# Performance work log

Hardware: AMD Instinct MI355X
Metric: run time of the kernel (lower is better)

The kernel has to match this reference:

```python
import jax, jax.numpy as jnp
import numpy as np

# LIFParameters(thr=0.4, tau=20.0, tau_o=20.0, damp=0.3, n_ref=5)
THR = 0.4
DECAY = float(np.exp(-1.0 / 20.0))   # membrane decay
KAPPA = float(np.exp(-1.0 / 20.0))   # output filter decay
N_REF = 5.0
DAMP = 0.3
SCALE = 1.0                           # scaling_factor

B, NIN, H, NOUT = 1024, 2048, 2048, 512


def setup_inputs() -> dict:
    key = jax.random.key(0)
    ks = jax.random.split(key, 10)
    inputs = (jax.random.uniform(ks[0], (B, NIN)) < 0.1).astype(jnp.float32)   # input spikes
    v = jax.random.uniform(ks[1], (B, H)) * THR                                # membrane potentials
    z = (jax.random.uniform(ks[2], (B, H)) < 0.2).astype(jnp.float32)          # previous spikes
    r = jax.random.randint(ks[3], (B, H), 0, 6).astype(jnp.float32)            # refractory counters
    out = jax.random.normal(ks[4], (B, NOUT)) * 0.1                            # filtered output
    trace_in = jax.random.uniform(ks[5], (B, NIN))
    trace_rec = jax.random.uniform(ks[6], (B, H))
    w_in = jax.random.normal(ks[7], (NIN, H)) / np.sqrt(NIN)
    w_rec = jax.random.normal(ks[8], (H, H)) / np.sqrt(H)
    w_out = jax.random.normal(ks[9], (H, NOUT)) / np.sqrt(H)
    return dict(inputs=inputs, v=v, z=z, r=r, out=out, trace_in=trace_in,
                trace_rec=trace_rec, w_in=w_in, w_rec=w_rec, w_out=w_out)


@jax.custom_vjp
def spike(v_scaled):
    return (v_scaled > 0.0).astype(v_scaled.dtype)

def _spike_fwd(v_scaled):
    return spike(v_scaled), v_scaled

def _spike_bwd(v_scaled, g):
    # surrogate gradient: damp * max(0, 1 - |v_scaled|)
    return (g * DAMP * jnp.maximum(1.0 - jnp.abs(v_scaled), 0.0),)

spike.defvjp(_spike_fwd, _spike_bwd)


def reference(inputs, v, z, r, out, trace_in, trace_rec, w_in, w_rec, w_out):
    # --- lif_step ---
    i_t = inputs @ w_in + z @ w_rec                      # [B,H] synaptic current
    new_v = DECAY * v + i_t - z * THR                    # leaky integration + reset
    v_scaled = (new_v - THR) / THR
    new_z = spike(v_scaled)
    new_z = jnp.where(r > 0.1, 0.0, new_z)               # refractory masking (old r)
    new_r = jnp.clip(r + N_REF * new_z - 1.0, 0.0, N_REF)
    new_out = KAPPA * out + new_z @ (w_out * SCALE)      # [B,NOUT]
    # --- e-prop extras (call_eprop) ---
    dz_dh = jnp.maximum(DAMP * (1.0 - jnp.abs(v_scaled)), 0.0) / THR
    dz_dh = jnp.where(r > 0.1, 0.0, dz_dh)               # zero in refractory period
    new_trace_in = trace_in * DECAY + inputs
    new_trace_rec = trace_rec * DECAY + z
    return (new_out, new_z, new_v, new_r, new_trace_in, new_trace_rec, dz_dh)
```

## Files before the change

### kernel.cpp

```cpp
#include <hip/hip_runtime.h>

#define Bq 1024
#define Hq 2048
#define NOUTq 512

#define DECAYF 0.95122942450071400910f
#define THRF 0.4f
#define SINVF 5931641.0f

#define OFF_OUT  0
#define OFF_Z    524288
#define OFF_V    2621440
#define OFF_R    4718592
#define OFF_TIN  6815744
#define OFF_TREC 8912896
#define OFF_DZ   11010048

#define WS_A     0ul
#define WS_Q0    4194304ul
#define WS_Q1    12582912ul
#define WS_Q2    20971520ul
#define WS_WOUTT 29360128ul
#define WS_P     31457280ul
#define WS_Z2    65011712ul
#define WS_NEED  69206016ul

typedef __attribute__((ext_vector_type(8))) short  bf16x8;
typedef __attribute__((ext_vector_type(4))) short  s16x4;
typedef __attribute__((ext_vector_type(4))) float  f32x4;
typedef __attribute__((ext_vector_type(4))) int    i32x4;
typedef __attribute__((ext_vector_type(4))) char   c8x4;

__device__ __forceinline__ unsigned short cvt_bf16(float f) {
  unsigned u = __float_as_uint(f);
  return (unsigned short)((u + 0x7FFFu + ((u >> 16) & 1u)) >> 16);
}

__device__ __forceinline__ void gl_lds16(const void* g, void* l) {
  __builtin_amdgcn_global_load_lds((const __attribute__((address_space(1))) unsigned int*)g,
                                   (__attribute__((address_space(3))) unsigned int*)l, 16, 0, 0);
}


__global__ __launch_bounds__(256)
void prep(const float* __restrict__ w_in, const float* __restrict__ w_rec,
          const float* __restrict__ w_out, signed char* __restrict__ Q0,
          signed char* __restrict__ Q1, signed char* __restrict__ Q2,
          short* __restrict__ WoutT,
          const f32x4* __restrict__ ins, const f32x4* __restrict__ zin,
          signed char* __restrict__ Acomb)
{
  __shared__ float tile[64][65];
  const int bx = blockIdx.x, tid = threadIdx.x;
  if (bx >= 2304) {
    const int i = (bx - 2304) * 256 + tid;
    const f32x4 b = ins[i];
    const f32x4 d = zin[i];
    const int e = i * 4, m = e >> 11, k = e & 2047;
    c8x4 ab, zb;
#pragma unroll
    for (int j = 0; j < 4; ++j) { ab[j] = (char)(b[j] != 0.0f); zb[j] = (char)(d[j] != 0.0f); }
    *(c8x4*)&Acomb[m * 4096 + k] = ab;
    *(c8x4*)&Acomb[m * 4096 + 2048 + k] = zb;
    return;
  }
  const int rr = tid >> 4, c4 = (tid & 15) * 4;
  if (bx < 2048) {
    const int k0 = (bx >> 5) * 64, n0 = (bx & 31) * 64;
#pragma unroll
    for (int p = 0; p < 4; ++p) {
      const int kk = p * 16 + rr, kg = k0 + kk;
      const float* src = (kg < 2048) ? &w_in[kg * 2048 + n0 + c4]
                                     : &w_rec[(kg - 2048) * 2048 + n0 + c4];
      const f32x4 v = *(const f32x4*)src;
#pragma unroll
      for (int j = 0; j < 4; ++j) tile[kk][c4 + j] = v[j];
    }
    __syncthreads();
#pragma unroll
    for (int p = 0; p < 4; ++p) {
      const int nn = p * 16 + rr;
      c8x4 b0, b1, b2;
#pragma unroll
      for (int j = 0; j < 4; ++j) {
        int q = __float2int_rn(tile[c4 + j][nn] * SINVF);
        const int d2 = ((q + 64) & 127) - 64;  q = (q - d2) >> 7;
        const int d1 = ((q + 64) & 127) - 64;  q = (q - d1) >> 7;
        b2[j] = (char)d2; b1[j] = (char)d1; b0[j] = (char)q;
      }
      const long off = (long)(n0 + nn) * 4096 + k0 + c4;
      *(c8x4*)&Q0[off] = b0;
      *(c8x4*)&Q1[off] = b1;
      *(c8x4*)&Q2[off] = b2;
    }
  } else {
    const int b2 = bx - 2048;
    const int k0 = (b2 >> 3) * 64, n0 = (b2 & 7) * 64;
#pragma unroll
    for (int p = 0; p < 4; ++p) {
      const int kk = p * 16 + rr;
      const f32x4 v = *(const f32x4*)&w_out[(k0 + kk) * 512 + n0 + c4];
#pragma unroll
      for (int j = 0; j < 4; ++j) tile[kk][c4 + j] = v[j];
    }
    __syncthreads();
#pragma unroll
    for (int p = 0; p < 4; ++p) {
      const int nn = p * 16 + rr;
      s16x4 hh;
#pragma unroll
      for (int j = 0; j < 4; ++j) hh[j] = (short)cvt_bf16(tile[c4 + j][nn]);
      *(s16x4*)&WoutT[(n0 + nn) * 2048 + k0 + c4] = hh;
    }
  }
}

__global__ __launch_bounds__(256, 2)
void gemm1(const signed char* __restrict__ Ag, const signed char* __restrict__ Q0g,
           const signed char* __restrict__ Q1g, const signed char* __restrict__ Q2g,
           int* __restrict__ outp)
{
  constexpr int KT = 8;
  __shared__ __align__(16) signed char As[128 * 128];
  __shared__ __align__(16) signed char B0[128 * 128];
  __shared__ __align__(16) signed char B1[128 * 128];
  __shared__ __align__(16) signed char B2[128 * 128];

  const int tid = threadIdx.x, lane = tid & 63, wv = tid >> 6;
  const int lr = lane & 15, hl = lane >> 4;
  const int r8 = lane >> 3, ts = lane & 7;

  const int bid = blockIdx.x;
  const int swz = (bid & 7) * 64 + (bid >> 3);
  const int m0 = (swz & 7) * 128;
  const int n0 = ((swz >> 3) & 15) * 128;
  const int kz = swz >> 7;
  const int kb = kz * 1024;
  int* P = outp + (size_t)kz * (Bq * Hq);

  const int wm = (wv >> 1) * 64;
  const int wn = (wv & 1) * 64;

  i32x4 a0[4][4], a1[4][4], a2[4][4];
#pragma unroll
  for (int mi = 0; mi < 4; ++mi)
#pragma unroll
    for (int ni = 0; ni < 4; ++ni) {
      a0[mi][ni] = (i32x4){0, 0, 0, 0};
      a1[mi][ni] = (i32x4){0, 0, 0, 0};
      a2[mi][ni] = (i32x4){0, 0, 0, 0};
    }

  auto STAGE = [&](int kt) {
    const int k = kb + kt * 128;
#pragma unroll
    for (int q = 0; q < 4; ++q) {
      const int slot = wv * 4 + q;
      const int r = slot * 8 + r8;
      const int s = ts ^ (r & 7);
      gl_lds16(Ag + (size_t)(m0 + r) * 4096 + k + s * 16, &As[slot * 1024]);
      gl_lds16(Q0g + (size_t)(n0 + r) * 4096 + k + s * 16, &B0[slot * 1024]);
      gl_lds16(Q1g + (size_t)(n0 + r) * 4096 + k + s * 16, &B1[slot * 1024]);
      gl_lds16(Q2g + (size_t)(n0 + r) * 4096 + k + s * 16, &B2[slot * 1024]);
    }
  };

  STAGE(0);
  for (int kt = 0; kt < KT; ++kt) {
    __syncthreads();
#pragma unroll
    for (int ks = 0; ks < 2; ++ks) {
      i32x4 af[4];
#pragma unroll
      for (int mi = 0; mi < 4; ++mi) {
        const int ar = wm + mi * 16 + lr;
        af[mi] = *(const i32x4*)&As[ar * 128 + (((ks * 4 + hl) ^ (ar & 7)) << 4)];
      }
#pragma unroll
      for (int ni = 0; ni < 4; ++ni) {
        const int br = wn + ni * 16 + lr;
        const int sp = (((ks * 4 + hl) ^ (br & 7)) << 4);
        const i32x4 b0 = *(const i32x4*)&B0[br * 128 + sp];
#pragma unroll
        for (int mi = 0; mi < 4; ++mi)
          a0[mi][ni] = __builtin_amdgcn_mfma_i32_16x16x64_i8(af[mi], b0, a0[mi][ni], 0, 0, 0);
        const i32x4 b1 = *(const i32x4*)&B1[br * 128 + sp];
#pragma unroll
        for (int mi = 0; mi < 4; ++mi)
          a1[mi][ni] = __builtin_amdgcn_mfma_i32_16x16x64_i8(af[mi], b1, a1[mi][ni], 0, 0, 0);
        const i32x4 b2 = *(const i32x4*)&B2[br * 128 + sp];
#pragma unroll
        for (int mi = 0; mi < 4; ++mi)
          a2[mi][ni] = __builtin_amdgcn_mfma_i32_16x16x64_i8(af[mi], b2, a2[mi][ni], 0, 0, 0);
      }
    }
    __syncthreads();
    if (kt + 1 < KT) STAGE(kt + 1);
  }

#pragma unroll
  for (int mi = 0; mi < 4; ++mi)
#pragma unroll
    for (int ni = 0; ni < 4; ++ni)
#pragma unroll
      for (int j = 0; j < 4; ++j) {
        const int m = m0 + wm + mi * 16 + hl * 4 + j;
        const int n = n0 + wn + ni * 16 + lr;
        P[m * Hq + n] = (a0[mi][ni][j] << 14) + (a1[mi][ni][j] << 7) + a2[mi][ni][j];
      }
}

__global__ __launch_bounds__(256)
void lif_epi(const i32x4* __restrict__ Pp, const f32x4* __restrict__ vin,
             const f32x4* __restrict__ zin, const f32x4* __restrict__ rin,
             float* __restrict__ dout, short* __restrict__ z2)
{
  const int i = blockIdx.x * 256 + threadIdx.x;
  const i32x4 c = Pp[i] + Pp[i + 524288] + Pp[i + 2 * 524288] + Pp[i + 3 * 524288];
  const double S = 1.0 / (double)SINVF;
  const f32x4 vo = vin[i], zo = zin[i], ro = rin[i];
  f32x4 nv, nz, nr, dz;
  s16x4 zb;
#pragma unroll
  for (int j = 0; j < 4; ++j) {
    const float it = (float)((double)c[j] * S);
    const float v1 = DECAYF * vo[j] + it - zo[j] * THRF;
    const float vs = (v1 - THRF) / THRF;
    const bool refr = ro[j] > 0.1f;
    const float z1 = (refr || !(vs > 0.0f)) ? 0.0f : 1.0f;
    nv[j] = v1; nz[j] = z1;
    nr[j] = fminf(fmaxf(ro[j] + 5.0f * z1 - 1.0f, 0.0f), 5.0f);
    dz[j] = refr ? 0.0f : (fmaxf(0.3f * (1.0f - fabsf(vs)), 0.0f) / THRF);
    zb[j] = (short)cvt_bf16(z1);
  }
  ((f32x4*)(dout + OFF_V))[i] = nv;
  ((f32x4*)(dout + OFF_Z))[i] = nz;
  ((f32x4*)(dout + OFF_R))[i] = nr;
  ((f32x4*)(dout + OFF_DZ))[i] = dz;
  ((s16x4*)z2)[i] = zb;
}

__global__ __launch_bounds__(256)
void tail(const short* __restrict__ Ag, const short* __restrict__ Whg,
          const float* __restrict__ e0, float* __restrict__ outp,
          const f32x4* __restrict__ tin, const f32x4* __restrict__ ins,
          const f32x4* __restrict__ trec, const f32x4* __restrict__ zin,
          f32x4* __restrict__ o1, f32x4* __restrict__ o2)
{
  constexpr int BM = 32, BN = 64, MR = 1, NR = 2, KT = 32, AK = 2048;
  constexpr int APW = BM / 32, WPW = BN / 32;
  __shared__ __align__(16) short As[BM * 64];
  __shared__ __align__(16) short Wh[BN * 64];

  const int bid = blockIdx.x, tid = threadIdx.x;
  if (bid >= 256) {
    const int i = (bid - 256) * 256 + tid;
    o1[i] = tin[i] * DECAYF + ins[i];
    o2[i] = trec[i] * DECAYF + zin[i];
    return;
  }
  const int lane = tid & 63, wv = tid >> 6;
  const int lr = lane & 15, hl = lane >> 4;
  const int rA = lane >> 3, ts = lane & 7;
  const int m0 = (bid >> 3) * BM, n0 = (bid & 7) * BN;
  const int wm = (wv >> 1) * (MR * 16);
  const int wn = (wv & 1) * (NR * 16);

  f32x4 acc[MR][NR];
#pragma unroll
  for (int mi = 0; mi < MR; ++mi)
#pragma unroll
    for (int ni = 0; ni < NR; ++ni) acc[mi][ni] = (f32x4){0.f, 0.f, 0.f, 0.f};

  auto STAGE = [&](int kt) {
    const int k = kt * 64;
#pragma unroll
    for (int q = 0; q < APW; ++q) {
      const int slot = wv * APW + q;
      const int r = slot * 8 + rA;
      const int s = ts ^ (r & 7);
      gl_lds16(Ag + (m0 + r) * AK + k + s * 8, &As[slot * 512]);
    }
#pragma unroll
    for (int q = 0; q < WPW; ++q) {
      const int slot = wv * WPW + q;
      const int r = slot * 8 + rA;
      const int s = ts ^ (r & 7);
      gl_lds16(Whg + (n0 + r) * AK + k + s * 8, &Wh[slot * 512]);
    }
  };

  STAGE(0);
  for (int kt = 0; kt < KT; ++kt) {
    __syncthreads();
#pragma unroll
    for (int ks = 0; ks < 2; ++ks) {
      bf16x8 af[MR];
#pragma unroll
      for (int mi = 0; mi < MR; ++mi) {
        const int r = wm + mi * 16 + lr;
        af[mi] = *(const bf16x8*)&As[r * 64 + (((ks * 4 + hl) ^ (r & 7)) << 3)];
      }
#pragma unroll
      for (int ni = 0; ni < NR; ++ni) {
        const int rn = wn + ni * 16 + lr;
        const int sp = (((ks * 4 + hl) ^ (rn & 7)) << 3);
        const bf16x8 bh = *(const bf16x8*)&Wh[rn * 64 + sp];
#pragma unroll
        for (int mi = 0; mi < MR; ++mi)
          acc[mi][ni] = __builtin_amdgcn_mfma_f32_16x16x32_bf16(af[mi], bh, acc[mi][ni], 0, 0, 0);
      }
    }
    __syncthreads();
    if (kt + 1 < KT) STAGE(kt + 1);
  }

#pragma unroll
  for (int mi = 0; mi < MR; ++mi)
#pragma unroll
    for (int ni = 0; ni < NR; ++ni)
#pragma unroll
      for (int j = 0; j < 4; ++j) {
        const int m = m0 + wm + mi * 16 + hl * 4 + j;
        const int n = n0 + wn + ni * 16 + lr;
        const int idx = m * NOUTq + n;
        outp[idx] = DECAYF * e0[idx] + acc[mi][ni][j];
      }
}


template<int MODE>
__global__ __launch_bounds__(256, 1)
void fb_gemm(const float* __restrict__ A0g, const float* __restrict__ A1g,
             const float* __restrict__ W0g, const float* __restrict__ W1g,
             const float* __restrict__ e0, const float* __restrict__ e1,
             const float* __restrict__ e2, float* __restrict__ dout)
{
  constexpr int BM = (MODE == 0) ? 64 : 32;
  constexpr int BN = (MODE == 0) ? 128 : 64;
  constexpr int BK = 64;
  constexpr int LDA = BK + 8;
  constexpr int MR = (MODE == 0) ? 2 : 1;
  constexpr int NR = (MODE == 0) ? 4 : 2;
  constexpr int WM = MR * 16, WN = NR * 16;
  constexpr int KT = (MODE == 0) ? 64 : 32;
  constexpr int Nmat = (MODE == 0) ? Hq : NOUTq;
  constexpr int QA = BM / 16;
  constexpr int QW = (16 * BN) / 256;
  constexpr int KSH = (MODE == 0) ? 7 : 6;
  constexpr int KSTEP = (MODE == 0) ? 2 : 4;

  __shared__ __align__(16) short As[BM * LDA];
  __shared__ __align__(16) short Wh[BN * LDA];
  __shared__ __align__(16) short Wl[((MODE == 0) ? BN : 1) * LDA];

  const int tid  = threadIdx.x;
  const int lane = tid & 63;
  const int wave = tid >> 6;
  const int lr = lane & 15, hl = lane >> 4;
  const int wmOff = (wave >> 1) * WM;
  const int wnOff = (wave & 1) * WN;
  const int m0 = blockIdx.y * BM;
  const int n0 = blockIdx.x * BN;
  const int arow = tid >> 4, ac4 = tid & 15;
  const int wn = tid & (BN - 1);

  f32x4 aR[QA];
  float wR[QW][4];
  f32x4 acc[MR][NR];
#pragma unroll
  for (int mi = 0; mi < MR; ++mi)
#pragma unroll
    for (int ni = 0; ni < NR; ++ni)
      acc[mi][ni] = (f32x4){0.f, 0.f, 0.f, 0.f};

  auto LOAD = [&](int kt) {
    const float* Ag = A0g; const float* Wg = W0g; int k0 = kt * BK;
    if (MODE == 0 && kt >= 32) { Ag = A1g; Wg = W1g; k0 = (kt - 32) * BK; }
#pragma unroll
    for (int q = 0; q < QA; ++q)
      aR[q] = *(const f32x4*)&Ag[(m0 + arow + q * 16) * 2048 + k0 + ac4 * 4];
#pragma unroll
    for (int p = 0; p < QW; ++p) {
      const int kq = (tid >> KSH) + p * KSTEP;
#pragma unroll
      for (int i = 0; i < 4; ++i)
        wR[p][i] = Wg[(k0 + kq * 4 + i) * Nmat + n0 + wn];
    }
  };

  auto STORE = [&]() {
#pragma unroll
    for (int q = 0; q < QA; ++q) {
      s16x4 hv;
#pragma unroll
      for (int j = 0; j < 4; ++j) hv[j] = (short)cvt_bf16(aR[q][j]);
      *(s16x4*)&As[(arow + q * 16) * LDA + ac4 * 4] = hv;
    }
#pragma unroll
    for (int p = 0; p < QW; ++p) {
      const int kq = (tid >> KSH) + p * KSTEP;
      s16x4 hh, ll;
#pragma unroll
      for (int i = 0; i < 4; ++i) {
        const float w = wR[p][i];
        const unsigned short h = cvt_bf16(w);
        hh[i] = (short)h;
        if (MODE == 0) {
          const float hf = __uint_as_float(((unsigned)h) << 16);
          ll[i] = (short)cvt_bf16(w - hf);
        }
      }
      *(s16x4*)&Wh[wn * LDA + kq * 4] = hh;
      if (MODE == 0) *(s16x4*)&Wl[wn * LDA + kq * 4] = ll;
    }
  };

  LOAD(0);
  for (int kt = 0; kt < KT; ++kt) {
    __syncthreads();
    STORE();
    __syncthreads();
    if (kt + 1 < KT) LOAD(kt + 1);
#pragma unroll
    for (int ks = 0; ks < 2; ++ks) {
      bf16x8 af[MR];
#pragma unroll
      for (int mi = 0; mi < MR; ++mi)
        af[mi] = *(const bf16x8*)&As[(wmOff + mi * 16 + lr) * LDA + ks * 32 + hl * 8];
#pragma unroll
      for (int ni = 0; ni < NR; ++ni) {
        const bf16x8 bh = *(const bf16x8*)&Wh[(wnOff + ni * 16 + lr) * LDA + ks * 32 + hl * 8];
#pragma unroll
        for (int mi = 0; mi < MR; ++mi)
          acc[mi][ni] = __builtin_amdgcn_mfma_f32_16x16x32_bf16(af[mi], bh, acc[mi][ni], 0, 0, 0);
        if (MODE == 0) {
          const bf16x8 bl = *(const bf16x8*)&Wl[(wnOff + ni * 16 + lr) * LDA + ks * 32 + hl * 8];
#pragma unroll
          for (int mi = 0; mi < MR; ++mi)
            acc[mi][ni] = __builtin_amdgcn_mfma_f32_16x16x32_bf16(af[mi], bl, acc[mi][ni], 0, 0, 0);
        }
      }
    }
  }

#pragma unroll
  for (int mi = 0; mi < MR; ++mi) {
#pragma unroll
    for (int ni = 0; ni < NR; ++ni) {
#pragma unroll
      for (int j = 0; j < 4; ++j) {
        const int m = m0 + wmOff + mi * 16 + hl * 4 + j;
        const int n = n0 + wnOff + ni * 16 + lr;
        if (MODE == 0) {
          const int idx = m * Hq + n;
          const float it = acc[mi][ni][j];
          const float vold = e0[idx];
          const float zold = e1[idx];
          const float rold = e2[idx];
          const float nv = DECAYF * vold + it - zold * THRF;
          const float vs = (nv - THRF) / THRF;
          const bool refr = rold > 0.1f;
          const float nz = (refr || !(vs > 0.0f)) ? 0.0f : 1.0f;
          const float nr = fminf(fmaxf(rold + 5.0f * nz - 1.0f, 0.0f), 5.0f);
          const float dz = refr ? 0.0f : (fmaxf(0.3f * (1.0f - fabsf(vs)), 0.0f) / THRF);
          dout[OFF_V + idx] = nv;
          dout[OFF_Z + idx] = nz;
          dout[OFF_R + idx] = nr;
          dout[OFF_DZ + idx] = dz;
        } else {
          const int idx = m * NOUTq + n;
          dout[OFF_OUT + idx] = DECAYF * e0[idx] + acc[mi][ni][j];
        }
      }
    }
  }
}

__global__ __launch_bounds__(256)
void fb_trace(const float4* __restrict__ tin, const float4* __restrict__ ins,
              const float4* __restrict__ trec, const float4* __restrict__ zin,
              float4* __restrict__ o1, float4* __restrict__ o2)
{
  const int n4 = (Bq * 2048) / 4;
  for (int i = blockIdx.x * blockDim.x + threadIdx.x; i < n4; i += gridDim.x * blockDim.x) {
    const float4 a = tin[i], b = ins[i];
    float4 u;
    u.x = a.x * DECAYF + b.x; u.y = a.y * DECAYF + b.y;
    u.z = a.z * DECAYF + b.z; u.w = a.w * DECAYF + b.w;
    o1[i] = u;
    const float4 c = trec[i], d = zin[i];
    float4 w;
    w.x = c.x * DECAYF + d.x; w.y = c.y * DECAYF + d.y;
    w.z = c.z * DECAYF + d.z; w.w = c.w * DECAYF + d.w;
    o2[i] = w;
  }
}

extern "C" void kernel_launch(void* const* d_in, const int* in_sizes, int n_in,
                              void* d_out, int out_size, void* d_ws, size_t ws_size,
                              hipStream_t stream) {
  const float* inputs = (const float*)d_in[0];
  const float* v      = (const float*)d_in[1];
  const float* z      = (const float*)d_in[2];
  const float* r      = (const float*)d_in[3];
  const float* outp   = (const float*)d_in[4];
  const float* tin    = (const float*)d_in[5];
  const float* trec   = (const float*)d_in[6];
  const float* w_in   = (const float*)d_in[7];
  const float* w_rec  = (const float*)d_in[8];
  const float* w_out  = (const float*)d_in[9];
  float* out = (float*)d_out;

  if (ws_size >= WS_NEED) {
    char* ws = (char*)d_ws;
    signed char* A  = (signed char*)(ws + WS_A);
    signed char* Q0 = (signed char*)(ws + WS_Q0);
    signed char* Q1 = (signed char*)(ws + WS_Q1);
    signed char* Q2 = (signed char*)(ws + WS_Q2);
    short* WoutT    = (short*)(ws + WS_WOUTT);
    int* P          = (int*)(ws + WS_P);
    short* Z2       = (short*)(ws + WS_Z2);

    prep<<<4352, 256, 0, stream>>>(w_in, w_rec, w_out, Q0, Q1, Q2, WoutT,
                                   (const f32x4*)inputs, (const f32x4*)z, A);
    gemm1<<<512, 256, 0, stream>>>(A, Q0, Q1, Q2, P);
    lif_epi<<<2048, 256, 0, stream>>>((const i32x4*)P, (const f32x4*)v, (const f32x4*)z,
                                      (const f32x4*)r, out, Z2);
    tail<<<2304, 256, 0, stream>>>(Z2, WoutT, outp, out + OFF_OUT,
                                   (const f32x4*)tin, (const f32x4*)inputs,
                                   (const f32x4*)trec, (const f32x4*)z,
                                   (f32x4*)(out + OFF_TIN), (f32x4*)(out + OFF_TREC));
  } else {
    fb_trace<<<2048, 256, 0, stream>>>((const float4*)tin, (const float4*)inputs,
                                       (const float4*)trec, (const float4*)z,
                                       (float4*)(out + OFF_TIN), (float4*)(out + OFF_TREC));
    fb_gemm<0><<<dim3(16, 16), 256, 0, stream>>>(inputs, z, w_in, w_rec, v, z, r, out);
    fb_gemm<1><<<dim3(8, 32), 256, 0, stream>>>(out + OFF_Z, nullptr, w_out, nullptr,
                                                outp, nullptr, nullptr, out);
  }
}
```

Before: 88.85 us.

## Double-buffer gemm1 LDS tiles with 512-thread blocks and explicit waitcnt pipelining

Reworks the int8 GEMM kernel so two K-tiles are staged into LDS ahead of use, with hand-placed vmcnt/lgkmcnt waits and raw barriers, overlapping global-to-LDS loads with MFMA compute. The block grows to 512 threads (8 waves, each owning a 32x64 output sub-tile) and runs one block per CU, using 128KB of LDS. This is meant to hide load latency that the single-buffered loop exposed, at the cost of lower occupancy and reliance on a correct vmcnt count (8 outstanding loads per stage).

```diff
diff --git a/kernel.cpp b/kernel.cpp
--- a/kernel.cpp
+++ b/kernel.cpp
@@ -30,6 +30,12 @@
 typedef __attribute__((ext_vector_type(4))) float  f32x4;
 typedef __attribute__((ext_vector_type(4))) int    i32x4;
 typedef __attribute__((ext_vector_type(4))) char   c8x4;
+
+#define VMCNT8  asm volatile("s_waitcnt vmcnt(8)" ::: "memory")
+#define VMCNT0  asm volatile("s_waitcnt vmcnt(0)" ::: "memory")
+#define LGKM0   asm volatile("s_waitcnt lgkmcnt(0)" ::: "memory")
+#define SB0     __builtin_amdgcn_sched_barrier(0)
+#define BARRAW  __builtin_amdgcn_s_barrier()
 
 __device__ __forceinline__ unsigned short cvt_bf16(float f) {
   unsigned u = __float_as_uint(f);
@@ -115,16 +121,13 @@
   }
 }
 
-__global__ __launch_bounds__(256, 2)
+__global__ __launch_bounds__(512, 1)
 void gemm1(const signed char* __restrict__ Ag, const signed char* __restrict__ Q0g,
            const signed char* __restrict__ Q1g, const signed char* __restrict__ Q2g,
            int* __restrict__ outp)
 {
   constexpr int KT = 8;
-  __shared__ __align__(16) signed char As[128 * 128];
-  __shared__ __align__(16) signed char B0[128 * 128];
-  __shared__ __align__(16) signed char B1[128 * 128];
-  __shared__ __align__(16) signed char B2[128 * 128];
+  __shared__ __align__(16) signed char L[2][4][16384];
 
   const int tid = threadIdx.x, lane = tid & 63, wv = tid >> 6;
   const int lr = lane & 15, hl = lane >> 4;
@@ -138,12 +141,12 @@
   const int kb = kz * 1024;
   int* P = outp + (size_t)kz * (Bq * Hq);
 
-  const int wm = (wv >> 1) * 64;
-  const int wn = (wv & 1) * 64;
-
-  i32x4 a0[4][4], a1[4][4], a2[4][4];
-#pragma unroll
-  for (int mi = 0; mi < 4; ++mi)
+  const int wm = (wv & 3) * 32;
+  const int wn = (wv >> 2) * 64;
+
+  i32x4 a0[2][4], a1[2][4], a2[2][4];
+#pragma unroll
+  for (int mi = 0; mi < 2; ++mi)
 #pragma unroll
     for (int ni = 0; ni < 4; ++ni) {
       a0[mi][ni] = (i32x4){0, 0, 0, 0};
@@ -151,55 +154,63 @@
       a2[mi][ni] = (i32x4){0, 0, 0, 0};
     }
 
-  auto STAGE = [&](int kt) {
+  auto STAGE = [&](int kt, int c) {
     const int k = kb + kt * 128;
 #pragma unroll
-    for (int q = 0; q < 4; ++q) {
-      const int slot = wv * 4 + q;
+    for (int q = 0; q < 2; ++q) {
+      const int slot = wv * 2 + q;
       const int r = slot * 8 + r8;
       const int s = ts ^ (r & 7);
-      gl_lds16(Ag + (size_t)(m0 + r) * 4096 + k + s * 16, &As[slot * 1024]);
-      gl_lds16(Q0g + (size_t)(n0 + r) * 4096 + k + s * 16, &B0[slot * 1024]);
-      gl_lds16(Q1g + (size_t)(n0 + r) * 4096 + k + s * 16, &B1[slot * 1024]);
-      gl_lds16(Q2g + (size_t)(n0 + r) * 4096 + k + s * 16, &B2[slot * 1024]);
+      const size_t go = (size_t)r * 4096 + k + s * 16;
+      gl_lds16(Ag  + (size_t)m0 * 4096 + go, &L[c][0][slot * 1024]);
+      gl_lds16(Q0g + (size_t)n0 * 4096 + go, &L[c][1][slot * 1024]);
+      gl_lds16(Q1g + (size_t)n0 * 4096 + go, &L[c][2][slot * 1024]);
+      gl_lds16(Q2g + (size_t)n0 * 4096 + go, &L[c][3][slot * 1024]);
     }
   };
 
-  STAGE(0);
-  for (int kt = 0; kt < KT; ++kt) {
-    __syncthreads();
+  auto COMPUTE = [&](int c) {
 #pragma unroll
     for (int ks = 0; ks < 2; ++ks) {
-      i32x4 af[4];
-#pragma unroll
-      for (int mi = 0; mi < 4; ++mi) {
+      i32x4 af[2];
+#pragma unroll
+      for (int mi = 0; mi < 2; ++mi) {
         const int ar = wm + mi * 16 + lr;
-        af[mi] = *(const i32x4*)&As[ar * 128 + (((ks * 4 + hl) ^ (ar & 7)) << 4)];
+        af[mi] = *(const i32x4*)&L[c][0][ar * 128 + (((ks * 4 + hl) ^ (ar & 7)) << 4)];
       }
 #pragma unroll
       for (int ni = 0; ni < 4; ++ni) {
         const int br = wn + ni * 16 + lr;
-        const int sp = (((ks * 4 + hl) ^ (br & 7)) << 4);
-        const i32x4 b0 = *(const i32x4*)&B0[br * 128 + sp];
-#pragma unroll
-        for (int mi = 0; mi < 4; ++mi)
+        const int sp = br * 128 + (((ks * 4 + hl) ^ (br & 7)) << 4);
+        const i32x4 b0 = *(const i32x4*)&L[c][1][sp];
+#pragma unroll
+        for (int mi = 0; mi < 2; ++mi)
           a0[mi][ni] = __builtin_amdgcn_mfma_i32_16x16x64_i8(af[mi], b0, a0[mi][ni], 0, 0, 0);
-        const i32x4 b1 = *(const i32x4*)&B1[br * 128 + sp];
-#pragma unroll
-        for (int mi = 0; mi < 4; ++mi)
+        const i32x4 b1 = *(const i32x4*)&L[c][2][sp];
+#pragma unroll
+        for (int mi = 0; mi < 2; ++mi)
           a1[mi][ni] = __builtin_amdgcn_mfma_i32_16x16x64_i8(af[mi], b1, a1[mi][ni], 0, 0, 0);
-        const i32x4 b2 = *(const i32x4*)&B2[br * 128 + sp];
-#pragma unroll
-        for (int mi = 0; mi < 4; ++mi)
+        const i32x4 b2 = *(const i32x4*)&L[c][3][sp];
+#pragma unroll
+        for (int mi = 0; mi < 2; ++mi)
           a2[mi][ni] = __builtin_amdgcn_mfma_i32_16x16x64_i8(af[mi], b2, a2[mi][ni], 0, 0, 0);
       }
     }
-    __syncthreads();
-    if (kt + 1 < KT) STAGE(kt + 1);
-  }
-
-#pragma unroll
-  for (int mi = 0; mi < 4; ++mi)
+  };
+
+  STAGE(0, 0);
+  STAGE(1, 1);
+  for (int kt = 0; kt < KT - 1; ++kt) {
+    VMCNT8; SB0; BARRAW; SB0;
+    COMPUTE(kt & 1);
+    LGKM0; SB0; BARRAW; SB0;
+    if (kt + 2 < KT) STAGE(kt + 2, kt & 1);
+  }
+  VMCNT0; SB0; BARRAW; SB0;
+  COMPUTE((KT - 1) & 1);
+
+#pragma unroll
+  for (int mi = 0; mi < 2; ++mi)
 #pragma unroll
     for (int ni = 0; ni < 4; ++ni)
 #pragma unroll
@@ -524,7 +535,7 @@
 
     prep<<<4352, 256, 0, stream>>>(w_in, w_rec, w_out, Q0, Q1, Q2, WoutT,
                                    (const f32x4*)inputs, (const f32x4*)z, A);
-    gemm1<<<512, 256, 0, stream>>>(A, Q0, Q1, Q2, P);
+    gemm1<<<512, 512, 0, stream>>>(A, Q0, Q1, Q2, P);
     lif_epi<<<2048, 256, 0, stream>>>((const i32x4*)P, (const f32x4*)v, (const f32x4*)z,
                                       (const f32x4*)r, out, Z2);
     tail<<<2304, 256, 0, stream>>>(Z2, WoutT, outp, out + OFF_OUT,
```

Result: faster. 85.12 us (-4.2%).
